# Kernel tuning notes

Measured on AMD Instinct MI355X. Metric: run time of the kernel, lower is better.

The kernel has to match this reference:

```python
import jax, jax.numpy as jnp
import numpy as np

NC, NPR, E, B = 200000, 100000, 500000, 200000
DIN, HID, HEADS = 16, 256, 8
D = HID // HEADS
NCOLOR, NSIZE, NGROUP = 1000, 30, 50


def setup_inputs() -> dict:
    key = jax.random.key(0)
    ks = jax.random.split(key, 24)
    g = lambda i, shape, s=0.05: jax.random.normal(ks[i], shape, jnp.float32) * s
    return dict(
        customer_x=g(0, (NC, DIN), 1.0),
        product_x=g(1, (NPR, DIN), 1.0),
        proj_cust_W=g(2, (DIN, HID)), proj_cust_b=jnp.zeros((HID,), jnp.float32),
        proj_prod_W=g(3, (DIN, HID)), proj_prod_b=jnp.zeros((HID,), jnp.float32),
        att_src_r=g(4, (HEADS, D)), att_dst_r=g(5, (HEADS, D)),
        att_src_rb=g(6, (HEADS, D)), att_dst_rb=g(7, (HEADS, D)),
        q_sem=g(8, (HID,)), k_lin_W=g(9, (HID, HID)), k_lin_b=jnp.zeros((HID,), jnp.float32),
        color_emb=g(10, (NCOLOR, 8), 1.0),
        size_emb=g(11, (NSIZE, 4), 1.0),
        group_emb=g(12, (NGROUP, 4), 1.0),
        fc1_W=g(13, (HID * 2 + 16, 128)), fc1_b=jnp.zeros((128,), jnp.float32),
        fc2_W=g(14, (128, 32)), fc2_b=jnp.zeros((32,), jnp.float32),
        fc3_W=g(15, (32, 1)), fc3_b=jnp.zeros((1,), jnp.float32),
        bn1_gamma=jnp.ones((128,), jnp.float32), bn1_beta=jnp.zeros((128,), jnp.float32),
        bn2_gamma=jnp.ones((32,), jnp.float32), bn2_beta=jnp.zeros((32,), jnp.float32),
        edge_src=jax.random.randint(ks[16], (E,), 0, NC),
        edge_dst=jax.random.randint(ks[17], (E,), 0, NPR),
        label_src=jax.random.randint(ks[18], (B,), 0, NC),
        label_dst=jax.random.randint(ks[19], (B,), 0, NPR),
        size_idx=jax.random.randint(ks[20], (B,), 0, NSIZE),
        color_idx=jax.random.randint(ks[21], (B,), 0, NCOLOR),
        group_idx=jax.random.randint(ks[22], (B,), 0, NGROUP),
    )


def _edge_softmax(logits, dst, n):
    # destination-grouped softmax over edges; logits: [E,H]
    m = jax.ops.segment_max(logits, dst, num_segments=n)
    m = jnp.where(jnp.isfinite(m), m, 0.0)
    e = jnp.exp(logits - m[dst])
    s = jax.ops.segment_sum(e, dst, num_segments=n)
    return e / (s[dst] + 1e-16)


def _han_relation(h_src, h_dst, a_src, a_dst, src, dst, n_dst):
    # h_*: [N,H,D]; a_*: [H,D]
    logits = (h_src * a_src).sum(-1)[src] + (h_dst * a_dst).sum(-1)[dst]  # [E,H]
    logits = jax.nn.leaky_relu(logits, 0.2)
    alpha = _edge_softmax(logits, dst, n_dst)
    msg = alpha[:, :, None] * h_src[src]  # [E,H,D]
    out = jax.ops.segment_sum(msg, dst, num_segments=n_dst)
    return jax.nn.relu(out.reshape(n_dst, -1))  # [N_dst, H*D]


def _group(outs, q, kW, kb):
    # semantic attention over metapaths (PyG HANConv group)
    stk = jnp.stack(outs)  # [M,N,F]
    score = (q * jnp.tanh(stk @ kW + kb).mean(1)).sum(-1)  # [M]
    attn = jax.nn.softmax(score)
    return jnp.einsum('m,mnf->nf', attn, stk)


def _bn(x, gamma, beta):
    mu = x.mean(0)
    var = x.var(0)
    return (x - mu) * jax.lax.rsqrt(var + 1e-5) * gamma + beta


def reference(customer_x, product_x, proj_cust_W, proj_cust_b, proj_prod_W, proj_prod_b,
              att_src_r, att_dst_r, att_src_rb, att_dst_rb, q_sem, k_lin_W, k_lin_b,
              color_emb, size_emb, group_emb, fc1_W, fc1_b, fc2_W, fc2_b, fc3_W, fc3_b,
              bn1_gamma, bn1_beta, bn2_gamma, bn2_beta,
              edge_src, edge_dst, label_src, label_dst, size_idx, color_idx, group_idx):
    h_c = (customer_x @ proj_cust_W + proj_cust_b).reshape(-1, HEADS, D)
    h_p = (product_x @ proj_prod_W + proj_prod_b).reshape(-1, HEADS, D)
    # relation customer -returns-> product
    out_p = _han_relation(h_c, h_p, att_src_r, att_dst_r, edge_src, edge_dst, NPR)
    # relation product -returned_by-> customer (reversed edges)
    out_c = _han_relation(h_p, h_c, att_src_rb, att_dst_rb, edge_dst, edge_src, NC)
    cust = _group([out_c], q_sem, k_lin_W, k_lin_b)  # [NC, 256]
    prod = _group([out_p], q_sem, k_lin_W, k_lin_b)  # [NPR, 256]
    feat = jnp.concatenate([cust[label_src], prod[label_dst],
                            size_emb[size_idx], color_emb[color_idx], group_emb[group_idx]], axis=-1)
    x = jax.nn.relu(feat @ fc1_W + fc1_b)
    x = _bn(x, bn1_gamma, bn1_beta)
    x = jax.nn.relu(x @ fc2_W + fc2_b)
    x = _bn(x, bn2_gamma, bn2_beta)
    return x @ fc3_W + fc3_b
```

## Files before the change

### kernel.cpp

```cpp
#include <hip/hip_runtime.h>

#define NCC 200000
#define NPRR 100000
#define NEE 500000
#define NBB 200000

typedef __attribute__((ext_vector_type(8))) short bf16x8;
typedef __attribute__((ext_vector_type(16))) float f32x16;

__device__ __forceinline__ float b2f(unsigned short u){ return __uint_as_float(((unsigned)u)<<16); }
__device__ __forceinline__ unsigned short f2b(float f){
  unsigned x = __float_as_uint(f);
  return (unsigned short)((x + 0x7fffu + ((x>>16)&1u)) >> 16);
}
__device__ __forceinline__ void gl2lds16(const void* g, void* l){
  __builtin_amdgcn_global_load_lds(
      (const __attribute__((address_space(1))) unsigned int*)g,
      (__attribute__((address_space(3))) unsigned int*)l, 16, 0, 0);
}

__global__ __launch_bounds__(256) void wa_prep2(
    const float* __restrict__ Wc, const float* __restrict__ bc,
    const float* __restrict__ attAc, const float* __restrict__ attBc,
    const float* __restrict__ Wp, const float* __restrict__ bp,
    const float* __restrict__ attAp, const float* __restrict__ attBp,
    float* __restrict__ WAc, float* __restrict__ WAp)
{
  int tid = threadIdx.x;
  for (int task = tid; task < 4*17*8; task += 256) {
    int grp = task / 136, rem = task % 136;
    int k = rem >> 3, h = rem & 7;
    const float* att = (grp==0)?attAc:(grp==1)?attBc:(grp==2)?attAp:attBp;
    const float* W   = (grp<2)?Wc:Wp;
    const float* bias= (grp<2)?bc:bp;
    const float* row = (k < 16) ? (W + k*256) : bias;
    float acc = 0.f;
    for (int d = 0; d < 32; d++) acc = fmaf(row[h*32+d], att[h*32+d], acc);
    if (grp<2) WAc[(grp&1)*136 + rem] = acc;
    else       WAp[(grp&1)*136 + rem] = acc;
  }
}

__global__ __launch_bounds__(256) void prep_proj(
    const float* __restrict__ Wc, const float* __restrict__ Wp,
    const float* __restrict__ WAc, const float* __restrict__ WAp,
    unsigned short* __restrict__ WtC, unsigned short* __restrict__ WtP,
    unsigned short* __restrict__ WAtC, unsigned short* __restrict__ WAtP)
{
  int idx = blockIdx.x*256 + threadIdx.x;
  if (idx < 4096){ int n=idx>>4, k=idx&15; WtC[idx]=f2b(Wc[k*256+n]); }
  else if (idx < 8192){ int t=idx-4096; int n=t>>4, k=t&15; WtP[t]=f2b(Wp[k*256+n]); }
  else if (idx < 8704){ int t=idx-8192; int n=t>>4, k=t&15;
    WAtC[t] = (n<16)? f2b(WAc[(n>>3)*136 + k*8 + (n&7)]) : (unsigned short)0; }
  else if (idx < 9216){ int t=idx-8704; int n=t>>4, k=t&15;
    WAtP[t] = (n<16)? f2b(WAp[(n>>3)*136 + k*8 + (n&7)]) : (unsigned short)0; }
}

__global__ __launch_bounds__(256) void prep_fc1(const float* __restrict__ fc1W,
    const float* __restrict__ fc1b,
    const float* __restrict__ size_emb, const float* __restrict__ color_emb,
    const float* __restrict__ group_emb,
    unsigned short* __restrict__ BtC, unsigned short* __restrict__ BtP,
    float* __restrict__ Ts, float* __restrict__ Tc, float* __restrict__ Tg)
{
  int idx = blockIdx.x*256 + threadIdx.x;
  if (idx < 32768){
    int n = idx>>8, k = idx&255;
    BtC[idx] = f2b(fc1W[k*128 + n]);
  } else if (idx < 65536){
    int t = idx - 32768;
    int n = t>>8, k = t&255;
    BtP[t] = f2b(fc1W[(256+k)*128 + n]);
  } else if (idx < 65536 + 30*128){
    int t = idx - 65536;
    int s = t>>7, j = t&127;
    float a = fc1b[j];
    #pragma unroll
    for (int c=0;c<4;c++) a = fmaf(size_emb[s*4+c], fc1W[(512+c)*128+j], a);
    Ts[t] = a;
  } else if (idx < 65536 + 30*128 + 1000*128){
    int t = idx - 65536 - 30*128;
    int col = t>>7, j = t&127;
    float a = 0.f;
    #pragma unroll
    for (int c=0;c<8;c++) a = fmaf(color_emb[col*8+c], fc1W[(516+c)*128+j], a);
    Tc[t] = a;
  } else if (idx < 65536 + 30*128 + 1000*128 + 50*128){
    int t = idx - 65536 - 30*128 - 1000*128;
    int g = t>>7, j = t&127;
    float a = 0.f;
    #pragma unroll
    for (int c=0;c<4;c++) a = fmaf(group_emb[g*4+c], fc1W[(524+c)*128+j], a);
    Tg[t] = a;
  }
}

__global__ __launch_bounds__(256) void proj_mfma(const float* __restrict__ X,
    const unsigned short* __restrict__ Wt, const unsigned short* __restrict__ WAt,
    const float* __restrict__ WA,
    unsigned short* __restrict__ H, float* __restrict__ sA, float* __restrict__ sB,
    int N, int nt)
{
  __shared__ unsigned short wt[4608];
  __shared__ float biasS[16];
  int tid = threadIdx.x;
  for (int i=tid; i<512; i+=256) ((uint4*)wt)[i] = ((const uint4*)Wt)[i];
  for (int i=tid; i<64;  i+=256) ((uint4*)(wt+4096))[i] = ((const uint4*)WAt)[i];
  if (tid < 16) biasS[tid] = WA[(tid>>3)*136 + 128 + (tid&7)];
  __syncthreads();
  int wv = tid>>6, lane = tid&63, m = lane&31, hi = lane>>5;
  for (int t = blockIdx.x; t < nt; t += gridDim.x){
    int node = t*32 + m;
    bf16x8 a;
    {
      const float4* xr = (const float4*)(X + (long long)node*16 + hi*8);
      float4 f0 = xr[0], f1 = xr[1];
      unsigned short av[8] = {f2b(f0.x),f2b(f0.y),f2b(f0.z),f2b(f0.w),
                              f2b(f1.x),f2b(f1.y),f2b(f1.z),f2b(f1.w)};
      a = *(bf16x8*)av;
    }
    #pragma unroll
    for (int s=0;s<2;s++){
      int c0 = wv*64 + s*32;
      bf16x8 b = *(const bf16x8*)(wt + (c0+m)*16 + hi*8);
      f32x16 acc;
      #pragma unroll
      for (int i=0;i<16;i++) acc[i]=0.f;
      acc = __builtin_amdgcn_mfma_f32_32x32x16_bf16(a, b, acc, 0, 0, 0);
      #pragma unroll
      for (int reg=0; reg<16; reg++){
        int row = (reg&3) + 8*(reg>>2) + 4*hi;
        H[(long long)(t*32+row)*256 + c0 + m] = f2b(acc[reg]);
      }
    }
    if (wv == 0){
      bf16x8 b = *(const bf16x8*)(wt + 4096 + m*16 + hi*8);
      f32x16 acc;
      #pragma unroll
      for (int i=0;i<16;i++) acc[i]=0.f;
      acc = __builtin_amdgcn_mfma_f32_32x32x16_bf16(a, b, acc, 0, 0, 0);
      if (m < 16){
        float bias = biasS[m];
        float* dst = (m < 8) ? sA : sB;
        int h = m & 7;
        #pragma unroll
        for (int reg=0; reg<16; reg++){
          int row = (reg&3) + 8*(reg>>2) + 4*hi;
          dst[(long long)(t*32+row)*8 + h] = acc[reg] + bias;
        }
      }
    }
  }
}

__global__ __launch_bounds__(256) void hist2(const int* __restrict__ src, const int* __restrict__ dst,
    int* __restrict__ cnt_c, int* __restrict__ cnt_p, int E)
{
  int e = blockIdx.x*256 + threadIdx.x;
  if (e >= E) return;
  atomicAdd(&cnt_p[dst[e]], 1);
  atomicAdd(&cnt_c[src[e]], 1);
}

__global__ __launch_bounds__(256) void scan_phase1(const int* __restrict__ cnt, int* __restrict__ bsum, int N)
{
  __shared__ int red[256];
  int tid = threadIdx.x;
  int base = blockIdx.x*1024 + tid*4;
  int s = 0;
  #pragma unroll
  for (int k=0;k<4;k++){ int i=base+k; if (i<N) s += cnt[i]; }
  red[tid] = s;
  __syncthreads();
  for (int off=128; off>0; off>>=1){ if (tid<off) red[tid]+=red[tid+off]; __syncthreads(); }
  if (tid==0) bsum[blockIdx.x] = red[0];
}

__global__ __launch_bounds__(256) void scan_phase2(int* __restrict__ bsum, int B,
    int* __restrict__ rowptr, int N)
{
  __shared__ int ts[256];
  int tid = threadIdx.x;
  int v = (tid<B) ? bsum[tid] : 0;
  ts[tid] = v;
  __syncthreads();
  for (int off=1; off<256; off<<=1){
    int t = (tid>=off) ? ts[tid-off] : 0;
    __syncthreads();
    ts[tid] += t;
    __syncthreads();
  }
  if (tid < B) bsum[tid] = ts[tid] - v;
  if (tid == B-1) rowptr[N] = ts[tid];
}

__global__ __launch_bounds__(256) void scan_phase3(const int* __restrict__ cnt,
    const int* __restrict__ bsum, int* __restrict__ rowptr, int N)
{
  __shared__ int ts[256];
  int tid = threadIdx.x;
  int base = blockIdx.x*1024 + tid*4;
  int v[4]; int s = 0;
  #pragma unroll
  for (int k=0;k<4;k++){ int i=base+k; v[k] = (i<N) ? cnt[i] : 0; s += v[k]; }
  ts[tid] = s;
  __syncthreads();
  for (int off=1; off<256; off<<=1){
    int t = (tid>=off) ? ts[tid-off] : 0;
    __syncthreads();
    ts[tid] += t;
    __syncthreads();
  }
  int run = bsum[blockIdx.x] + ts[tid] - s;
  #pragma unroll
  for (int k=0;k<4;k++){ int i=base+k; if (i<N){ rowptr[i]=run; run += v[k]; } }
}

__global__ __launch_bounds__(256) void place2(const int* __restrict__ src, const int* __restrict__ dst,
    const int* __restrict__ rp_r, const int* __restrict__ rp_rb,
    int* __restrict__ cnt_p, int* __restrict__ cnt_c,
    int* __restrict__ si_r, int* __restrict__ si_rb, int E)
{
  int e = blockIdx.x*256 + threadIdx.x;
  if (e >= E) return;
  int s = src[e], d = dst[e];
  si_r [rp_r [d] + atomicAdd(&cnt_p[d], 1)] = s;
  si_rb[rp_rb[s] + atomicAdd(&cnt_c[s], 1)] = d;
}

__global__ __launch_bounds__(256) void agg_kernel(
    const int* __restrict__ rowptr, const int* __restrict__ srcidx,
    const float* __restrict__ sSrc, const float* __restrict__ sDst,
    const unsigned short* __restrict__ H, unsigned short* __restrict__ out, int N)
{
  int wv = threadIdx.x >> 6, lane = threadIdx.x & 63;
  int n = blockIdx.x*4 + wv;
  if (n >= N) return;
  int e0 = rowptr[n], e1 = rowptr[n+1];
  int j = lane & 31;
  int side = lane >> 5;
  int h = j >> 2;
  float sdh = sDst[(long long)n*8 + h];
  float a0=0,a1=0,a2=0,a3=0,a4=0,a5=0,a6=0,a7=0, da=0.f;
  float b0=0,b1=0,b2=0,b3=0,b4=0,b5=0,b6=0,b7=0, db=0.f;
  int e = e0 + side;
  for (; e + 2 < e1; e += 4){
    int sA = srcidx[e], sB = srcidx[e+2];
    float lA = sSrc[(long long)sA*8 + h] + sdh;
    float lB = sSrc[(long long)sB*8 + h] + sdh;
    uint4 uA = *(const uint4*)&H[(long long)sA*256 + j*8];
    uint4 uB = *(const uint4*)&H[(long long)sB*256 + j*8];
    float wA = __expf(lA > 0.f ? lA : 0.2f*lA);
    float wB = __expf(lB > 0.f ? lB : 0.2f*lB);
    da += wA; db += wB;
    a0 = fmaf(wA, b2f((unsigned short)(uA.x&0xffffu)), a0);
    a1 = fmaf(wA, b2f((unsigned short)(uA.x>>16)),     a1);
    a2 = fmaf(wA, b2f((unsigned short)(uA.y&0xffffu)), a2);
    a3 = fmaf(wA, b2f((unsigned short)(uA.y>>16)),     a3);
    a4 = fmaf(wA, b2f((unsigned short)(uA.z&0xffffu)), a4);
    a5 = fmaf(wA, b2f((unsigned short)(uA.z>>16)),     a5);
    a6 = fmaf(wA, b2f((unsigned short)(uA.w&0xffffu)), a6);
    a7 = fmaf(wA, b2f((unsigned short)(uA.w>>16)),     a7);
    b0 = fmaf(wB, b2f((unsigned short)(uB.x&0xffffu)), b0);
    b1 = fmaf(wB, b2f((unsigned short)(uB.x>>16)),     b1);
    b2 = fmaf(wB, b2f((unsigned short)(uB.y&0xffffu)), b2);
    b3 = fmaf(wB, b2f((unsigned short)(uB.y>>16)),     b3);
    b4 = fmaf(wB, b2f((unsigned short)(uB.z&0xffffu)), b4);
    b5 = fmaf(wB, b2f((unsigned short)(uB.z>>16)),     b5);
    b6 = fmaf(wB, b2f((unsigned short)(uB.w&0xffffu)), b6);
    b7 = fmaf(wB, b2f((unsigned short)(uB.w>>16)),     b7);
  }
  for (; e < e1; e += 2){
    int s = srcidx[e];
    float l = sSrc[(long long)s*8 + h] + sdh;
    uint4 u = *(const uint4*)&H[(long long)s*256 + j*8];
    float w = __expf(l > 0.f ? l : 0.2f*l);
    da += w;
    a0 = fmaf(w, b2f((unsigned short)(u.x&0xffffu)), a0);
    a1 = fmaf(w, b2f((unsigned short)(u.x>>16)),     a1);
    a2 = fmaf(w, b2f((unsigned short)(u.y&0xffffu)), a2);
    a3 = fmaf(w, b2f((unsigned short)(u.y>>16)),     a3);
    a4 = fmaf(w, b2f((unsigned short)(u.z&0xffffu)), a4);
    a5 = fmaf(w, b2f((unsigned short)(u.z>>16)),     a5);
    a6 = fmaf(w, b2f((unsigned short)(u.w&0xffffu)), a6);
    a7 = fmaf(w, b2f((unsigned short)(u.w>>16)),     a7);
  }
  a0+=b0; a1+=b1; a2+=b2; a3+=b3; a4+=b4; a5+=b5; a6+=b6; a7+=b7;
  da += db;
  a0 += __shfl_xor(a0,32); a1 += __shfl_xor(a1,32);
  a2 += __shfl_xor(a2,32); a3 += __shfl_xor(a3,32);
  a4 += __shfl_xor(a4,32); a5 += __shfl_xor(a5,32);
  a6 += __shfl_xor(a6,32); a7 += __shfl_xor(a7,32);
  da += __shfl_xor(da,32);
  float inv = 1.f/(da + 1e-16f);
  if (side == 0){
    uint4 o;
    o.x = (unsigned)f2b(fmaxf(a0*inv,0.f)) | ((unsigned)f2b(fmaxf(a1*inv,0.f))<<16);
    o.y = (unsigned)f2b(fmaxf(a2*inv,0.f)) | ((unsigned)f2b(fmaxf(a3*inv,0.f))<<16);
    o.z = (unsigned)f2b(fmaxf(a4*inv,0.f)) | ((unsigned)f2b(fmaxf(a5*inv,0.f))<<16);
    o.w = (unsigned)f2b(fmaxf(a6*inv,0.f)) | ((unsigned)f2b(fmaxf(a7*inv,0.f))<<16);
    *(uint4*)&out[(long long)n*256 + j*8] = o;
  }
}

__global__ __launch_bounds__(256) void gemmY(const unsigned short* __restrict__ A,
    const unsigned short* __restrict__ Bt, unsigned short* __restrict__ Y, int M)
{
  __shared__ unsigned short feat[32*264];
  int tid = threadIdx.x;
  int wv = tid>>6, lane = tid&63;
  long long base = (long long)blockIdx.x*32;
  #pragma unroll
  for (int i=0;i<8;i++){
    int r = wv*8 + i;
    if (lane < 32) gl2lds16(A + (base+r)*256 + lane*8, &feat[r*264]);
  }
  __syncthreads();
  int m = lane&31, hi = lane>>5;
  f32x16 acc;
  #pragma unroll
  for (int i=0;i<16;i++) acc[i]=0.f;
  const unsigned short* ap  = feat + m*264 + hi*8;
  const unsigned short* btp = Bt + (wv*32 + m)*256 + hi*8;
  #pragma unroll 4
  for (int ks=0; ks<16; ks++){
    bf16x8 a = *(const bf16x8*)(ap + ks*16);
    bf16x8 b = *(const bf16x8*)(btp + ks*16);
    acc = __builtin_amdgcn_mfma_f32_32x32x16_bf16(a, b, acc, 0, 0, 0);
  }
  int col = wv*32 + m;
  #pragma unroll
  for (int reg=0; reg<16; reg++){
    int row = (reg&3) + 8*(reg>>2) + 4*hi;
    Y[(base+row)*128 + col] = f2b(acc[reg]);
  }
}

__global__ __launch_bounds__(256) void gather_fc1(
    const unsigned short* __restrict__ Yc, const unsigned short* __restrict__ Yp,
    const float* __restrict__ Ts, const float* __restrict__ Tc, const float* __restrict__ Tg,
    const int* __restrict__ lsrc, const int* __restrict__ ldst,
    const int* __restrict__ sidx, const int* __restrict__ cidx, const int* __restrict__ gidx,
    unsigned short* __restrict__ x1, float* __restrict__ bnsum, int ntiles)
{
  __shared__ float redS[16][128];
  __shared__ float redQ[16][128];
  int tid = threadIdx.x;
  int rl = tid>>4, g = tid&15;
  float sacc[8] = {0,0,0,0,0,0,0,0};
  float qacc[8] = {0,0,0,0,0,0,0,0};
  for (int t = blockIdx.x; t < ntiles; t += gridDim.x){
    long long row = (long long)t*16 + rl;
    int ls = lsrc[row], ld = ldst[row], si = sidx[row], ci = cidx[row], gi = gidx[row];
    uint4 uc = *(const uint4*)&Yc[(long long)ls*128 + g*8];
    uint4 up = *(const uint4*)&Yp[(long long)ld*128 + g*8];
    float4 t0 = *(const float4*)&Ts[si*128 + g*8];
    float4 t1 = *(const float4*)&Ts[si*128 + g*8 + 4];
    float4 c0 = *(const float4*)&Tc[ci*128 + g*8];
    float4 c1 = *(const float4*)&Tc[ci*128 + g*8 + 4];
    float4 g0 = *(const float4*)&Tg[gi*128 + g*8];
    float4 g1 = *(const float4*)&Tg[gi*128 + g*8 + 4];
    unsigned ucs[4] = {uc.x,uc.y,uc.z,uc.w};
    unsigned ups[4] = {up.x,up.y,up.z,up.w};
    float tb[8] = {t0.x+c0.x+g0.x, t0.y+c0.y+g0.y, t0.z+c0.z+g0.z, t0.w+c0.w+g0.w,
                   t1.x+c1.x+g1.x, t1.y+c1.y+g1.y, t1.z+c1.z+g1.z, t1.w+c1.w+g1.w};
    unsigned short ov[8];
    #pragma unroll
    for (int p=0;p<4;p++){
      float vl = b2f((unsigned short)(ucs[p]&0xffffu)) + b2f((unsigned short)(ups[p]&0xffffu)) + tb[p*2];
      float vh = b2f((unsigned short)(ucs[p]>>16))     + b2f((unsigned short)(ups[p]>>16))     + tb[p*2+1];
      vl = fmaxf(vl, 0.f); vh = fmaxf(vh, 0.f);
      ov[p*2] = f2b(vl); ov[p*2+1] = f2b(vh);
      sacc[p*2]   += vl; qacc[p*2]   += vl*vl;
      sacc[p*2+1] += vh; qacc[p*2+1] += vh*vh;
    }
    *(uint4*)&x1[row*128 + g*8] = *(uint4*)ov;
  }
  #pragma unroll
  for (int j=0;j<8;j++){ redS[rl][g*8+j]=sacc[j]; redQ[rl][g*8+j]=qacc[j]; }
  __syncthreads();
  if (tid < 128){
    float s=0.f, q=0.f;
    #pragma unroll
    for (int r=0;r<16;r++){ s += redS[r][tid]; q += redQ[r][tid]; }
    atomicAdd(&bnsum[tid], s);
    atomicAdd(&bnsum[128+tid], q);
  }
}

__global__ void bn1_fold(const float* __restrict__ bnsum,
    const float* __restrict__ gamma, const float* __restrict__ beta,
    const float* __restrict__ fc2W, const float* __restrict__ fc2b,
    unsigned short* __restrict__ Bt2, float* __restrict__ b2p, float invB)
{
  __shared__ float sc[128], sh[128];
  int tid = threadIdx.x;
  if (tid<128){
    float mu  = bnsum[tid]*invB;
    float var = bnsum[128+tid]*invB - mu*mu;
    float s = gamma[tid] * rsqrtf(var + 1e-5f);
    sc[tid]=s; sh[tid]= beta[tid] - mu*s;
  }
  __syncthreads();
  for (int idx=tid; idx<32*128; idx+=256){
    int n = idx>>7, k = idx&127;
    Bt2[idx] = f2b(sc[k]*fc2W[k*32+n]);
  }
  if (tid<32){
    float a = fc2b[tid];
    for (int k=0;k<128;k++) a = fmaf(sh[k], fc2W[k*32+tid], a);
    b2p[tid]=a;
  }
}

__global__ __launch_bounds__(256) void fc2_mfma(const unsigned short* __restrict__ x1,
    const unsigned short* __restrict__ Bt2, const float* __restrict__ b2p,
    unsigned short* __restrict__ x2, float* __restrict__ bnsum2, int M)
{
  __shared__ unsigned short xt[128*136];
  __shared__ unsigned short wt[32*136];
  __shared__ float redS[4][32];
  __shared__ float redQ[4][32];
  int tid = threadIdx.x;
  long long base = (long long)blockIdx.x*128;
  for (int idx=tid; idx<128*16; idx+=256){
    int r = idx>>4, c = idx&15;
    uint4 u = make_uint4(0,0,0,0);
    if (base + r < M) u = *(const uint4*)&x1[(base+r)*128 + c*8];
    *(uint4*)&xt[r*136 + c*8] = u;
  }
  for (int idx=tid; idx<32*16; idx+=256){
    int r = idx>>4, c = idx&15;
    *(uint4*)&wt[r*136 + c*8] = *(const uint4*)&Bt2[r*128 + c*8];
  }
  __syncthreads();
  int wv = tid>>6, lane = tid&63;
  int m = lane&31, hi = lane>>5;
  f32x16 acc;
  #pragma unroll
  for (int i=0;i<16;i++) acc[i]=0.f;
  const unsigned short* ap = xt + (wv*32 + m)*136 + hi*8;
  const unsigned short* bp = wt + m*136 + hi*8;
  #pragma unroll
  for (int ks=0; ks<8; ks++){
    bf16x8 a = *(const bf16x8*)(ap + ks*16);
    bf16x8 b = *(const bf16x8*)(bp + ks*16);
    acc = __builtin_amdgcn_mfma_f32_32x32x16_bf16(a, b, acc, 0, 0, 0);
  }
  int col = m;
  float bias = b2p[col];
  float s=0.f, q=0.f;
  #pragma unroll
  for (int reg=0; reg<16; reg++){
    int row = (reg&3) + 8*(reg>>2) + 4*hi;
    long long grow = base + wv*32 + row;
    float v = fmaxf(acc[reg] + bias, 0.f);
    if (grow < M) x2[grow*32 + col] = f2b(v);
    s += v; q += v*v;
  }
  if (base + 128 > M){
    s = 0.f; q = 0.f;
    #pragma unroll
    for (int reg=0; reg<16; reg++){
      int row = (reg&3) + 8*(reg>>2) + 4*hi;
      long long grow = base + wv*32 + row;
      float v = fmaxf(acc[reg] + bias, 0.f);
      if (grow < M){ s += v; q += v*v; }
    }
  }
  s += __shfl_xor(s, 32);
  q += __shfl_xor(q, 32);
  if (hi == 0){ redS[wv][col] = s; redQ[wv][col] = q; }
  __syncthreads();
  if (tid < 32){
    float a = redS[0][tid]+redS[1][tid]+redS[2][tid]+redS[3][tid];
    float b = redQ[0][tid]+redQ[1][tid]+redQ[2][tid]+redQ[3][tid];
    atomicAdd(&bnsum2[tid], a);
    atomicAdd(&bnsum2[32+tid], b);
  }
}

__global__ void bn2_fold(const float* __restrict__ bnsum2,
    const float* __restrict__ gamma2, const float* __restrict__ beta2,
    const float* __restrict__ fc3W, const float* __restrict__ fc3b,
    float* __restrict__ w3p, float invB)
{
  __shared__ float sh3[32];
  int tid = threadIdx.x;
  if (tid<32){
    float mu  = bnsum2[tid]*invB;
    float var = bnsum2[32+tid]*invB - mu*mu;
    float s   = gamma2[tid] * rsqrtf(var + 1e-5f);
    float shv = beta2[tid] - mu*s;
    float w   = fc3W[tid];
    w3p[tid]  = s*w;
    sh3[tid]  = shv*w;
  }
  __syncthreads();
  if (tid==0){
    float a = fc3b[0];
    for (int j=0;j<32;j++) a += sh3[j];
    w3p[32] = a;
  }
}

__global__ __launch_bounds__(256) void fc3_kernel(const unsigned short* __restrict__ x2,
    const float* __restrict__ w3p, float* __restrict__ out)
{
  __shared__ float wl[34];
  int tid = threadIdx.x;
  if (tid<33) wl[tid]=w3p[tid];
  __syncthreads();
  long long row = (long long)blockIdx.x*32 + (tid>>3);
  int j0 = (tid&7)*4;
  uint2 u = *(const uint2*)(x2 + row*32 + j0);
  float a = b2f((unsigned short)(u.x&0xffffu))*wl[j0]
          + b2f((unsigned short)(u.x>>16))   *wl[j0+1]
          + b2f((unsigned short)(u.y&0xffffu))*wl[j0+2]
          + b2f((unsigned short)(u.y>>16))   *wl[j0+3];
  a += __shfl_xor(a,1);
  a += __shfl_xor(a,2);
  a += __shfl_xor(a,4);
  if ((tid&7)==0) out[row] = a + wl[32];
}

extern "C" void kernel_launch(void* const* d_in, const int* in_sizes, int n_in,
                              void* d_out, int out_size, void* d_ws, size_t ws_size,
                              hipStream_t stream)
{
  (void)in_sizes; (void)n_in; (void)out_size; (void)ws_size;
  const float* customer_x = (const float*)d_in[0];
  const float* product_x  = (const float*)d_in[1];
  const float* pcW = (const float*)d_in[2];
  const float* pcB = (const float*)d_in[3];
  const float* ppW = (const float*)d_in[4];
  const float* ppB = (const float*)d_in[5];
  const float* att_src_r  = (const float*)d_in[6];
  const float* att_dst_r  = (const float*)d_in[7];
  const float* att_src_rb = (const float*)d_in[8];
  const float* att_dst_rb = (const float*)d_in[9];
  const float* color_emb = (const float*)d_in[13];
  const float* size_emb  = (const float*)d_in[14];
  const float* group_emb = (const float*)d_in[15];
  const float* fc1W = (const float*)d_in[16];
  const float* fc1b = (const float*)d_in[17];
  const float* fc2W = (const float*)d_in[18];
  const float* fc2b = (const float*)d_in[19];
  const float* fc3W = (const float*)d_in[20];
  const float* fc3b = (const float*)d_in[21];
  const float* bn1g = (const float*)d_in[22];
  const float* bn1b = (const float*)d_in[23];
  const float* bn2g = (const float*)d_in[24];
  const float* bn2b = (const float*)d_in[25];
  const int* edge_src  = (const int*)d_in[26];
  const int* edge_dst  = (const int*)d_in[27];
  const int* label_src = (const int*)d_in[28];
  const int* label_dst = (const int*)d_in[29];
  const int* size_idx  = (const int*)d_in[30];
  const int* color_idx = (const int*)d_in[31];
  const int* group_idx = (const int*)d_in[32];

  char* ws = (char*)d_ws;
  size_t off = 0;
  auto alloc = [&](size_t bytes)->char* {
    char* p = ws + off;
    off += (bytes + 255) & ~(size_t)255;
    return p;
  };
  unsigned short* H_c  = (unsigned short*)alloc((size_t)NCC*256*2);
  unsigned short* H_p  = (unsigned short*)alloc((size_t)NPRR*256*2);
  unsigned short* out_p= (unsigned short*)alloc((size_t)NPRR*256*2);
  float* s_cr     = (float*)alloc((size_t)NCC*8*4);
  float* s_crb    = (float*)alloc((size_t)NCC*8*4);
  float* s_pr     = (float*)alloc((size_t)NPRR*8*4);
  float* s_prb    = (float*)alloc((size_t)NPRR*8*4);
  int* rowptr_r   = (int*)alloc((size_t)(NPRR+1)*4);
  int* rowptr_rb  = (int*)alloc((size_t)(NCC+1)*4);
  int* srcidx_r   = (int*)alloc((size_t)NEE*4);
  int* srcidx_rb  = (int*)alloc((size_t)NEE*4);
  int* cnts       = (int*)alloc((size_t)(NCC+NPRR)*2*4);
  int* cnt_c      = cnts;
  int* cnt_p      = cnts + NCC;
  int* cnt_c2     = cnts + NCC + NPRR;
  int* cnt_p2     = cnts + NCC + NPRR + NCC;
  int* bsum_c     = (int*)alloc(256*4);
  int* bsum_p     = (int*)alloc(256*4);
  unsigned short* BtC = (unsigned short*)alloc(128*256*2);
  unsigned short* BtP = (unsigned short*)alloc(128*256*2);
  float* Ts     = (float*)alloc(30*128*4);
  float* Tc     = (float*)alloc(1000*128*4);
  float* Tg     = (float*)alloc(50*128*4);
  float* wa_c   = (float*)alloc(272*4);
  float* wa_p   = (float*)alloc(272*4);
  unsigned short* WtC  = (unsigned short*)alloc(256*16*2);
  unsigned short* WtP  = (unsigned short*)alloc(256*16*2);
  unsigned short* WAtC = (unsigned short*)alloc(32*16*2);
  unsigned short* WAtP = (unsigned short*)alloc(32*16*2);
  float* bnsum1 = (float*)alloc(256*4);
  float* bnsum2 = (float*)alloc(64*4);
  unsigned short* Bt2 = (unsigned short*)alloc(32*128*2);
  float* b2p    = (float*)alloc(32*4);
  float* w3p    = (float*)alloc(34*4);
  unsigned short* out_c = H_c;
  unsigned short* Y_p   = H_p;
  unsigned short* Y_c   = out_p;
  unsigned short* x1b   = H_c;
  unsigned short* x2b   = (unsigned short*)s_cr;

  hipMemsetAsync(bnsum1, 0, 1280, stream);
  hipMemsetAsync(cnts, 0, (size_t)(NCC+NPRR)*2*4, stream);

  wa_prep2<<<1,256,0,stream>>>(pcW, pcB, att_src_r, att_dst_rb,
                               ppW, ppB, att_dst_r, att_src_rb, wa_c, wa_p);
  prep_proj<<<36,256,0,stream>>>(pcW, ppW, wa_c, wa_p, WtC, WtP, WAtC, WAtP);
  prep_fc1<<<(203776+255)/256,256,0,stream>>>(fc1W, fc1b, size_emb, color_emb, group_emb,
      BtC, BtP, Ts, Tc, Tg);

  proj_mfma<<<2048,256,0,stream>>>(customer_x, WtC, WAtC, wa_c, H_c, s_cr, s_crb, NCC, NCC/32);
  proj_mfma<<<2048,256,0,stream>>>(product_x,  WtP, WAtP, wa_p, H_p, s_pr, s_prb, NPRR, NPRR/32);

  const int eg = (NEE+255)/256;
  const int BP = (NPRR+1023)/1024;
  const int BC = (NCC +1023)/1024;
  hist2<<<eg,256,0,stream>>>(edge_src, edge_dst, cnt_c, cnt_p, NEE);
  scan_phase1<<<BP,256,0,stream>>>(cnt_p, bsum_p, NPRR);
  scan_phase2<<<1,256,0,stream>>>(bsum_p, BP, rowptr_r, NPRR);
  scan_phase3<<<BP,256,0,stream>>>(cnt_p, bsum_p, rowptr_r, NPRR);
  scan_phase1<<<BC,256,0,stream>>>(cnt_c, bsum_c, NCC);
  scan_phase2<<<1,256,0,stream>>>(bsum_c, BC, rowptr_rb, NCC);
  scan_phase3<<<BC,256,0,stream>>>(cnt_c, bsum_c, rowptr_rb, NCC);
  place2<<<eg,256,0,stream>>>(edge_src, edge_dst, rowptr_r, rowptr_rb,
      cnt_p2, cnt_c2, srcidx_r, srcidx_rb, NEE);

  agg_kernel<<<(NPRR+3)/4,256,0,stream>>>(rowptr_r,  srcidx_r,  s_cr,  s_pr,  H_c, out_p, NPRR);
  agg_kernel<<<(NCC +3)/4,256,0,stream>>>(rowptr_rb, srcidx_rb, s_prb, s_crb, H_p, out_c, NCC);

  gemmY<<<NPRR/32,256,0,stream>>>(out_p, BtP, Y_p, NPRR);
  gemmY<<<NCC/32,256,0,stream>>>(out_c, BtC, Y_c, NCC);
  gather_fc1<<<2048,256,0,stream>>>(Y_c, Y_p, Ts, Tc, Tg,
      label_src, label_dst, size_idx, color_idx, group_idx, x1b, bnsum1, NBB/16);

  bn1_fold<<<1,256,0,stream>>>(bnsum1, bn1g, bn1b, fc2W, fc2b, Bt2, b2p, 1.0f/NBB);
  fc2_mfma<<<(NBB+127)/128,256,0,stream>>>(x1b, Bt2, b2p, x2b, bnsum2, NBB);
  bn2_fold<<<1,64,0,stream>>>(bnsum2, bn2g, bn2b, fc3W, fc3b, w3p, 1.0f/NBB);
  fc3_kernel<<<NBB/32,256,0,stream>>>(x2b, w3p, (float*)d_out);
}
```

Baseline: 628.1 us.

## Fuse edge aggregation into the following MFMA projection GEMM via LDS

The attention-weighted neighbor aggregation now writes its bf16 rows straight into the shared-memory tile used by the MFMA GEMM, instead of going through a global intermediate buffer and a separate kernel. This removes a full write and re-read of the aggregated features for both relations, plus two kernel launches. Each wave now aggregates eight nodes sequentially before the GEMM, so gather parallelism per block drops and the GEMM waits on the slowest node's aggregation. Workspace aliasing is rearranged so the intermediate buffer is reused for outputs.

```diff
diff --git a/kernel.cpp b/kernel.cpp
--- a/kernel.cpp
+++ b/kernel.cpp
@@ -12,11 +12,6 @@
 __device__ __forceinline__ unsigned short f2b(float f){
   unsigned x = __float_as_uint(f);
   return (unsigned short)((x + 0x7fffu + ((x>>16)&1u)) >> 16);
-}
-__device__ __forceinline__ void gl2lds16(const void* g, void* l){
-  __builtin_amdgcn_global_load_lds(
-      (const __attribute__((address_space(1))) unsigned int*)g,
-      (__attribute__((address_space(3))) unsigned int*)l, 16, 0, 0);
 }
 
 __global__ __launch_bounds__(256) void wa_prep2(
@@ -228,92 +223,83 @@
   si_rb[rp_rb[s] + atomicAdd(&cnt_c[s], 1)] = d;
 }
 
-__global__ __launch_bounds__(256) void agg_kernel(
+__global__ __launch_bounds__(256) void agg_gemm(
     const int* __restrict__ rowptr, const int* __restrict__ srcidx,
     const float* __restrict__ sSrc, const float* __restrict__ sDst,
-    const unsigned short* __restrict__ H, unsigned short* __restrict__ out, int N)
-{
-  int wv = threadIdx.x >> 6, lane = threadIdx.x & 63;
-  int n = blockIdx.x*4 + wv;
-  if (n >= N) return;
-  int e0 = rowptr[n], e1 = rowptr[n+1];
-  int j = lane & 31;
-  int side = lane >> 5;
-  int h = j >> 2;
-  float sdh = sDst[(long long)n*8 + h];
-  float a0=0,a1=0,a2=0,a3=0,a4=0,a5=0,a6=0,a7=0, da=0.f;
-  float b0=0,b1=0,b2=0,b3=0,b4=0,b5=0,b6=0,b7=0, db=0.f;
-  int e = e0 + side;
-  for (; e + 2 < e1; e += 4){
-    int sA = srcidx[e], sB = srcidx[e+2];
-    float lA = sSrc[(long long)sA*8 + h] + sdh;
-    float lB = sSrc[(long long)sB*8 + h] + sdh;
-    uint4 uA = *(const uint4*)&H[(long long)sA*256 + j*8];
-    uint4 uB = *(const uint4*)&H[(long long)sB*256 + j*8];
-    float wA = __expf(lA > 0.f ? lA : 0.2f*lA);
-    float wB = __expf(lB > 0.f ? lB : 0.2f*lB);
-    da += wA; db += wB;
-    a0 = fmaf(wA, b2f((unsigned short)(uA.x&0xffffu)), a0);
-    a1 = fmaf(wA, b2f((unsigned short)(uA.x>>16)),     a1);
-    a2 = fmaf(wA, b2f((unsigned short)(uA.y&0xffffu)), a2);
-    a3 = fmaf(wA, b2f((unsigned short)(uA.y>>16)),     a3);
-    a4 = fmaf(wA, b2f((unsigned short)(uA.z&0xffffu)), a4);
-    a5 = fmaf(wA, b2f((unsigned short)(uA.z>>16)),     a5);
-    a6 = fmaf(wA, b2f((unsigned short)(uA.w&0xffffu)), a6);
-    a7 = fmaf(wA, b2f((unsigned short)(uA.w>>16)),     a7);
-    b0 = fmaf(wB, b2f((unsigned short)(uB.x&0xffffu)), b0);
-    b1 = fmaf(wB, b2f((unsigned short)(uB.x>>16)),     b1);
-    b2 = fmaf(wB, b2f((unsigned short)(uB.y&0xffffu)), b2);
-    b3 = fmaf(wB, b2f((unsigned short)(uB.y>>16)),     b3);
-    b4 = fmaf(wB, b2f((unsigned short)(uB.z&0xffffu)), b4);
-    b5 = fmaf(wB, b2f((unsigned short)(uB.z>>16)),     b5);
-    b6 = fmaf(wB, b2f((unsigned short)(uB.w&0xffffu)), b6);
-    b7 = fmaf(wB, b2f((unsigned short)(uB.w>>16)),     b7);
-  }
-  for (; e < e1; e += 2){
-    int s = srcidx[e];
-    float l = sSrc[(long long)s*8 + h] + sdh;
-    uint4 u = *(const uint4*)&H[(long long)s*256 + j*8];
-    float w = __expf(l > 0.f ? l : 0.2f*l);
-    da += w;
-    a0 = fmaf(w, b2f((unsigned short)(u.x&0xffffu)), a0);
-    a1 = fmaf(w, b2f((unsigned short)(u.x>>16)),     a1);
-    a2 = fmaf(w, b2f((unsigned short)(u.y&0xffffu)), a2);
-    a3 = fmaf(w, b2f((unsigned short)(u.y>>16)),     a3);
-    a4 = fmaf(w, b2f((unsigned short)(u.z&0xffffu)), a4);
-    a5 = fmaf(w, b2f((unsigned short)(u.z>>16)),     a5);
-    a6 = fmaf(w, b2f((unsigned short)(u.w&0xffffu)), a6);
-    a7 = fmaf(w, b2f((unsigned short)(u.w>>16)),     a7);
-  }
-  a0+=b0; a1+=b1; a2+=b2; a3+=b3; a4+=b4; a5+=b5; a6+=b6; a7+=b7;
-  da += db;
-  a0 += __shfl_xor(a0,32); a1 += __shfl_xor(a1,32);
-  a2 += __shfl_xor(a2,32); a3 += __shfl_xor(a3,32);
-  a4 += __shfl_xor(a4,32); a5 += __shfl_xor(a5,32);
-  a6 += __shfl_xor(a6,32); a7 += __shfl_xor(a7,32);
-  da += __shfl_xor(da,32);
-  float inv = 1.f/(da + 1e-16f);
-  if (side == 0){
-    uint4 o;
-    o.x = (unsigned)f2b(fmaxf(a0*inv,0.f)) | ((unsigned)f2b(fmaxf(a1*inv,0.f))<<16);
-    o.y = (unsigned)f2b(fmaxf(a2*inv,0.f)) | ((unsigned)f2b(fmaxf(a3*inv,0.f))<<16);
-    o.z = (unsigned)f2b(fmaxf(a4*inv,0.f)) | ((unsigned)f2b(fmaxf(a5*inv,0.f))<<16);
-    o.w = (unsigned)f2b(fmaxf(a6*inv,0.f)) | ((unsigned)f2b(fmaxf(a7*inv,0.f))<<16);
-    *(uint4*)&out[(long long)n*256 + j*8] = o;
-  }
-}
-
-__global__ __launch_bounds__(256) void gemmY(const unsigned short* __restrict__ A,
-    const unsigned short* __restrict__ Bt, unsigned short* __restrict__ Y, int M)
+    const unsigned short* __restrict__ H, const unsigned short* __restrict__ Bt,
+    unsigned short* __restrict__ Y)
 {
   __shared__ unsigned short feat[32*264];
   int tid = threadIdx.x;
   int wv = tid>>6, lane = tid&63;
+  int j = lane & 31, side = lane >> 5, h = j >> 2;
   long long base = (long long)blockIdx.x*32;
-  #pragma unroll
+  #pragma unroll 1
   for (int i=0;i<8;i++){
     int r = wv*8 + i;
-    if (lane < 32) gl2lds16(A + (base+r)*256 + lane*8, &feat[r*264]);
+    long long n = base + r;
+    int e0 = rowptr[n], e1 = rowptr[n+1];
+    float sdh = sDst[n*8 + h];
+    float a0=0,a1=0,a2=0,a3=0,a4=0,a5=0,a6=0,a7=0, da=0.f;
+    float b0=0,b1=0,b2=0,b3=0,b4=0,b5=0,b6=0,b7=0, db=0.f;
+    int e = e0 + side;
+    for (; e + 2 < e1; e += 4){
+      int sA = srcidx[e], sB = srcidx[e+2];
+      float lA = sSrc[(long long)sA*8 + h] + sdh;
+      float lB = sSrc[(long long)sB*8 + h] + sdh;
+      uint4 uA = *(const uint4*)&H[(long long)sA*256 + j*8];
+      uint4 uB = *(const uint4*)&H[(long long)sB*256 + j*8];
+      float wA = __expf(lA > 0.f ? lA : 0.2f*lA);
+      float wB = __expf(lB > 0.f ? lB : 0.2f*lB);
+      da += wA; db += wB;
+      a0 = fmaf(wA, b2f((unsigned short)(uA.x&0xffffu)), a0);
+      a1 = fmaf(wA, b2f((unsigned short)(uA.x>>16)),     a1);
+      a2 = fmaf(wA, b2f((unsigned short)(uA.y&0xffffu)), a2);
+      a3 = fmaf(wA, b2f((unsigned short)(uA.y>>16)),     a3);
+      a4 = fmaf(wA, b2f((unsigned short)(uA.z&0xffffu)), a4);
+      a5 = fmaf(wA, b2f((unsigned short)(uA.z>>16)),     a5);
+      a6 = fmaf(wA, b2f((unsigned short)(uA.w&0xffffu)), a6);
+      a7 = fmaf(wA, b2f((unsigned short)(uA.w>>16)),     a7);
+      b0 = fmaf(wB, b2f((unsigned short)(uB.x&0xffffu)), b0);
+      b1 = fmaf(wB, b2f((unsigned short)(uB.x>>16)),     b1);
+      b2 = fmaf(wB, b2f((unsigned short)(uB.y&0xffffu)), b2);
+      b3 = fmaf(wB, b2f((unsigned short)(uB.y>>16)),     b3);
+      b4 = fmaf(wB, b2f((unsigned short)(uB.z&0xffffu)), b4);
+      b5 = fmaf(wB, b2f((unsigned short)(uB.z>>16)),     b5);
+      b6 = fmaf(wB, b2f((unsigned short)(uB.w&0xffffu)), b6);
+      b7 = fmaf(wB, b2f((unsigned short)(uB.w>>16)),     b7);
+    }
+    for (; e < e1; e += 2){
+      int s = srcidx[e];
+      float l = sSrc[(long long)s*8 + h] + sdh;
+      uint4 u = *(const uint4*)&H[(long long)s*256 + j*8];
+      float w = __expf(l > 0.f ? l : 0.2f*l);
+      da += w;
+      a0 = fmaf(w, b2f((unsigned short)(u.x&0xffffu)), a0);
+      a1 = fmaf(w, b2f((unsigned short)(u.x>>16)),     a1);
+      a2 = fmaf(w, b2f((unsigned short)(u.y&0xffffu)), a2);
+      a3 = fmaf(w, b2f((unsigned short)(u.y>>16)),     a3);
+      a4 = fmaf(w, b2f((unsigned short)(u.z&0xffffu)), a4);
+      a5 = fmaf(w, b2f((unsigned short)(u.z>>16)),     a5);
+      a6 = fmaf(w, b2f((unsigned short)(u.w&0xffffu)), a6);
+      a7 = fmaf(w, b2f((unsigned short)(u.w>>16)),     a7);
+    }
+    a0+=b0; a1+=b1; a2+=b2; a3+=b3; a4+=b4; a5+=b5; a6+=b6; a7+=b7;
+    da += db;
+    a0 += __shfl_xor(a0,32); a1 += __shfl_xor(a1,32);
+    a2 += __shfl_xor(a2,32); a3 += __shfl_xor(a3,32);
+    a4 += __shfl_xor(a4,32); a5 += __shfl_xor(a5,32);
+    a6 += __shfl_xor(a6,32); a7 += __shfl_xor(a7,32);
+    da += __shfl_xor(da,32);
+    float inv = 1.f/(da + 1e-16f);
+    if (side == 0){
+      unsigned short ov[8];
+      ov[0]=f2b(fmaxf(a0*inv,0.f)); ov[1]=f2b(fmaxf(a1*inv,0.f));
+      ov[2]=f2b(fmaxf(a2*inv,0.f)); ov[3]=f2b(fmaxf(a3*inv,0.f));
+      ov[4]=f2b(fmaxf(a4*inv,0.f)); ov[5]=f2b(fmaxf(a5*inv,0.f));
+      ov[6]=f2b(fmaxf(a6*inv,0.f)); ov[7]=f2b(fmaxf(a7*inv,0.f));
+      *(uint4*)&feat[r*264 + j*8] = *(uint4*)ov;
+    }
   }
   __syncthreads();
   int m = lane&31, hi = lane>>5;
@@ -569,7 +555,7 @@
   };
   unsigned short* H_c  = (unsigned short*)alloc((size_t)NCC*256*2);
   unsigned short* H_p  = (unsigned short*)alloc((size_t)NPRR*256*2);
-  unsigned short* out_p= (unsigned short*)alloc((size_t)NPRR*256*2);
+  unsigned short* slab = (unsigned short*)alloc((size_t)NPRR*256*2);
   float* s_cr     = (float*)alloc((size_t)NCC*8*4);
   float* s_crb    = (float*)alloc((size_t)NCC*8*4);
   float* s_pr     = (float*)alloc((size_t)NPRR*8*4);
@@ -601,11 +587,10 @@
   unsigned short* Bt2 = (unsigned short*)alloc(32*128*2);
   float* b2p    = (float*)alloc(32*4);
   float* w3p    = (float*)alloc(34*4);
-  unsigned short* out_c = H_c;
-  unsigned short* Y_p   = H_p;
-  unsigned short* Y_c   = out_p;
-  unsigned short* x1b   = H_c;
-  unsigned short* x2b   = (unsigned short*)s_cr;
+  unsigned short* Y_p = slab;
+  unsigned short* Y_c = H_c;
+  unsigned short* x1b = H_p;
+  unsigned short* x2b = (unsigned short*)s_cr;
 
   hipMemsetAsync(bnsum1, 0, 1280, stream);
   hipMemsetAsync(cnts, 0, (size_t)(NCC+NPRR)*2*4, stream);
@@ -632,11 +617,9 @@
   place2<<<eg,256,0,stream>>>(edge_src, edge_dst, rowptr_r, rowptr_rb,
       cnt_p2, cnt_c2, srcidx_r, srcidx_rb, NEE);
 
-  agg_kernel<<<(NPRR+3)/4,256,0,stream>>>(rowptr_r,  srcidx_r,  s_cr,  s_pr,  H_c, out_p, NPRR);
-  agg_kernel<<<(NCC +3)/4,256,0,stream>>>(rowptr_rb, srcidx_rb, s_prb, s_crb, H_p, out_c, NCC);
-
-  gemmY<<<NPRR/32,256,0,stream>>>(out_p, BtP, Y_p, NPRR);
-  gemmY<<<NCC/32,256,0,stream>>>(out_c, BtC, Y_c, NCC);
+  agg_gemm<<<NPRR/32,256,0,stream>>>(rowptr_r,  srcidx_r,  s_cr,  s_pr,  H_c, BtP, Y_p);
+  agg_gemm<<<NCC/32,256,0,stream>>>(rowptr_rb, srcidx_rb, s_prb, s_crb, H_p, BtC, Y_c);
+
   gather_fc1<<<2048,256,0,stream>>>(Y_c, Y_p, Ts, Tc, Tg,
       label_src, label_dst, size_idx, color_idx, group_idx, x1b, bnsum1, NBB/16);
 
```

Result: faster. 612.2 us (-2.5%).
